# Kernel tuning notes

Measured on AMD Instinct MI355X. Metric: run time of the kernel, lower is better.

Reference implementation:

```python
import jax, jax.numpy as jnp
import numpy as np

N_CHARS = 256
EMB = 1024
HID = 2048
SEQ = 8192

def setup_inputs() -> dict:
    key = jax.random.key(0)
    ks = jax.random.split(key, 7)
    s = 0.02
    return {
        "input_seq": jax.random.randint(ks[0], (SEQ,), 0, N_CHARS),
        "emb": jax.random.normal(ks[1], (N_CHARS, EMB), jnp.float32) * s,
        "wax_w": jax.random.normal(ks[2], (HID, EMB), jnp.float32) * s,
        "wax_b": jnp.zeros((HID,), jnp.float32),
        "waa_w": jax.random.normal(ks[3], (HID, HID), jnp.float32) * s,
        "wya_w": jax.random.normal(ks[4], (N_CHARS, HID), jnp.float32) * s,
        "wya_b": jnp.zeros((N_CHARS,), jnp.float32),
    }

def reference(input_seq, emb, wax_w, wax_b, waa_w, wya_w, wya_b):
    # Embed whole sequence: [T, E]
    x_seq = emb[input_seq]
    # Precompute the input projection for all steps (parallel GEMM): [T, H]
    xa_seq = x_seq @ wax_w.T + wax_b

    def step(h, xa):
        h_new = jnp.tanh(xa + h @ waa_w.T)  # [H]
        o = h_new @ wya_w.T + wya_b          # [n_chars]
        return h_new, o

    h0 = jnp.zeros((HID,), x_seq.dtype)
    h_final, out = jax.lax.scan(step, h0, xa_seq)
    # out: [T, n_chars]; hidden returned as [1, H] to match torch module
    return out, h_final[None, :]
```

## Files before the change

### kernel.cpp

```cpp
#include <hip/hip_runtime.h>
#include <stdint.h>

#define SEQ 8192
#define EMB 1024
#define HID 2048
#define NCH 256

#define SCAN_B 128
#define SCAN_T 256
#define ROWS_PB (HID / SCAN_B)
#define SENT 0xFFFFFFFFu
#define NREP 4
#define NSLOT 8

typedef unsigned uint4v __attribute__((ext_vector_type(4)));

__global__ __launch_bounds__(256) void gemm_tn(const float* __restrict__ X,
                                               const float* __restrict__ W,
                                               const float* __restrict__ bias,
                                               float* __restrict__ C,
                                               int M, int N, int K)
{
    __shared__ float Xs[16][68];
    __shared__ float Ws[16][68];
    const int m0 = blockIdx.x * 64, n0 = blockIdx.y * 64;
    const int tid  = threadIdx.x;
    const int lrow = tid >> 2;
    const int kq   = (tid & 3) * 4;
    const int tx   = tid & 15, ty = tid >> 4;
    float acc[4][4] = {};
    const float* Xp = X + (size_t)(m0 + lrow) * K + kq;
    const float* Wp = W + (size_t)(n0 + lrow) * K + kq;

    for (int k0 = 0; k0 < K; k0 += 16) {
        float4 xv = *(const float4*)(Xp + k0);
        float4 wv = *(const float4*)(Wp + k0);
        __syncthreads();
        Xs[kq+0][lrow] = xv.x; Xs[kq+1][lrow] = xv.y;
        Xs[kq+2][lrow] = xv.z; Xs[kq+3][lrow] = xv.w;
        Ws[kq+0][lrow] = wv.x; Ws[kq+1][lrow] = wv.y;
        Ws[kq+2][lrow] = wv.z; Ws[kq+3][lrow] = wv.w;
        __syncthreads();
#pragma unroll
        for (int kk = 0; kk < 16; ++kk) {
            float4 av = *(const float4*)&Xs[kk][ty * 4];
            float4 bv = *(const float4*)&Ws[kk][tx * 4];
            float a[4] = {av.x, av.y, av.z, av.w};
            float b[4] = {bv.x, bv.y, bv.z, bv.w};
#pragma unroll
            for (int i = 0; i < 4; ++i)
#pragma unroll
                for (int j = 0; j < 4; ++j)
                    acc[i][j] += a[i] * b[j];
        }
    }
#pragma unroll
    for (int i = 0; i < 4; ++i) {
        const int m = m0 + ty * 4 + i;
#pragma unroll
        for (int j = 0; j < 4; ++j) {
            const int n = n0 + tx * 4 + j;
            C[(size_t)m * N + n] = acc[i][j] + bias[n];
        }
    }
}

__device__ __forceinline__ float fast_tanh(float x)
{
    float e = __builtin_amdgcn_exp2f(x * 2.885390081777927f);
    return 1.0f - 2.0f * __builtin_amdgcn_rcpf(e + 1.0f);
}

__global__ __launch_bounds__(SCAN_T, 1) void rnn_scan(
    const int*  __restrict__ seq,
    const float* __restrict__ waa,
    const float* __restrict__ P,
    float* __restrict__ H,
    unsigned* __restrict__ ring)
{
    const int b    = blockIdx.x;
    const int tid  = threadIdx.x;
    const int wv   = tid >> 6;
    const int lane = tid & 63;
    const int R0   = b * ROWS_PB + wv * 4;
    const int rep  = b & (NREP - 1);

    __shared__ float hbuf[2][HID];

    float w0[32], w1[32], w2[32], w3[32];
#pragma unroll
    for (int j = 0; j < 8; ++j) {
        const float* base = waa + 256 * j + 4 * lane;
        float4 a = *(const float4*)(base + (size_t)(R0 + 0) * HID);
        float4 c = *(const float4*)(base + (size_t)(R0 + 1) * HID);
        float4 d = *(const float4*)(base + (size_t)(R0 + 2) * HID);
        float4 e = *(const float4*)(base + (size_t)(R0 + 3) * HID);
        w0[4*j+0]=a.x; w0[4*j+1]=a.y; w0[4*j+2]=a.z; w0[4*j+3]=a.w;
        w1[4*j+0]=c.x; w1[4*j+1]=c.y; w1[4*j+2]=c.z; w1[4*j+3]=c.w;
        w2[4*j+0]=d.x; w2[4*j+1]=d.y; w2[4*j+2]=d.z; w2[4*j+3]=d.w;
        w3[4*j+0]=e.x; w3[4*j+1]=e.y; w3[4*j+2]=e.z; w3[4*j+3]=e.w;
    }
#pragma unroll
    for (int k = 0; k < 32; ++k) {
        asm volatile("" : "+v"(w0[k])); asm volatile("" : "+v"(w1[k]));
        asm volatile("" : "+v"(w2[k])); asm volatile("" : "+v"(w3[k]));
    }

    unsigned* myring = ring + (size_t)rep * NSLOT * HID;
    const uint4v SV = {SENT, SENT, SENT, SENT};
    uint4v v0 = SV, v1 = SV;

#pragma unroll 1
    for (int t = 0; t < SEQ; ++t) {
        const int ch = seq[t];
        float xav = 0.f;
        if (lane < 4) xav = P[(size_t)ch * HID + R0 + lane];

        asm volatile("s_waitcnt vmcnt(9)" : "+v"(v0), "+v"(v1) : : "memory");
        if (v0.x == SENT || v0.y == SENT || v0.z == SENT || v0.w == SENT ||
            v1.x == SENT || v1.y == SENT || v1.z == SENT || v1.w == SENT) {
            const unsigned* pp =
                myring + (size_t)(t & (NSLOT - 1)) * HID + tid * 8;
            do {
                asm volatile("s_waitcnt vmcnt(0)\n\t"
                             "global_load_dwordx4 %0, %2, off sc0 sc1\n\t"
                             "global_load_dwordx4 %1, %2, off offset:16 sc0 sc1\n\t"
                             "s_waitcnt vmcnt(0)"
                             : "+v"(v0), "+v"(v1) : "v"(pp) : "memory");
            } while (v0.x == SENT || v0.y == SENT || v0.z == SENT || v0.w == SENT ||
                     v1.x == SENT || v1.y == SENT || v1.z == SENT || v1.w == SENT);
        }
        *(uint4v*)&hbuf[t & 1][tid * 8]     = v0;
        *(uint4v*)&hbuf[t & 1][tid * 8 + 4] = v1;
        __syncthreads();

        float a0 = 0.f, a1 = 0.f, a2 = 0.f, a3 = 0.f;
        const float* hb = &hbuf[t & 1][4 * lane];
#pragma unroll
        for (int j = 0; j < 8; ++j) {
            float4 hv = *(const float4*)(hb + 256 * j);
            a0 += w0[4*j+0]*hv.x + w0[4*j+1]*hv.y + w0[4*j+2]*hv.z + w0[4*j+3]*hv.w;
            a1 += w1[4*j+0]*hv.x + w1[4*j+1]*hv.y + w1[4*j+2]*hv.z + w1[4*j+3]*hv.w;
            a2 += w2[4*j+0]*hv.x + w2[4*j+1]*hv.y + w2[4*j+2]*hv.z + w2[4*j+3]*hv.w;
            a3 += w3[4*j+0]*hv.x + w3[4*j+1]*hv.y + w3[4*j+2]*hv.z + w3[4*j+3]*hv.w;
        }
        a0 += __shfl_xor(a0, 1, 64);
        a1 += __shfl_xor(a1, 1, 64);
        a2 += __shfl_xor(a2, 1, 64);
        a3 += __shfl_xor(a3, 1, 64);
        float m01 = (lane & 1) ? a1 : a0;
        float m23 = (lane & 1) ? a3 : a2;
        m01 += __shfl_xor(m01, 2, 64);
        m23 += __shfl_xor(m23, 2, 64);
        float m = (lane & 2) ? m23 : m01;
        m += __shfl_xor(m, 4, 64);
        m += __shfl_xor(m, 8, 64);
        m += __shfl_xor(m, 16, 64);
        m += __shfl_xor(m, 32, 64);

        if (t + 1 < SEQ) {
            const unsigned* pn =
                myring + (size_t)((t + 1) & (NSLOT - 1)) * HID + tid * 8;
            v0 = SV; v1 = SV;
            asm volatile("global_load_dwordx4 %0, %2, off sc0 sc1\n\t"
                         "global_load_dwordx4 %1, %2, off offset:16 sc0 sc1"
                         : "+v"(v0), "+v"(v1) : "v"(pn) : "memory");
        }

        if (lane < 4) {
            float hn = fast_tanh(xav + m);
            const unsigned hu = __float_as_uint(hn);
            const int row = R0 + lane;
            const int s1 = (t + 1) & (NSLOT - 1);
            const int s5 = (t + 5) & (NSLOT - 1);
#pragma unroll
            for (int r = 0; r < NREP; ++r)
                __hip_atomic_store(ring + ((size_t)r * NSLOT + s1) * HID + row,
                                   hu, __ATOMIC_RELAXED,
                                   __HIP_MEMORY_SCOPE_AGENT);
#pragma unroll
            for (int r = 0; r < NREP; ++r)
                __hip_atomic_store(ring + ((size_t)r * NSLOT + s5) * HID + row,
                                   SENT, __ATOMIC_RELAXED,
                                   __HIP_MEMORY_SCOPE_AGENT);
            H[(size_t)(t + 1) * HID + row] = hn;
        }
    }
}

__global__ void copy_h(const float* __restrict__ src, float* __restrict__ dst)
{
    int i = blockIdx.x * blockDim.x + threadIdx.x;
    if (i < HID) dst[i] = src[i];
}

extern "C" void kernel_launch(void* const* d_in, const int* in_sizes, int n_in,
                              void* d_out, int out_size, void* d_ws, size_t ws_size,
                              hipStream_t stream)
{
    const int*   seq  = (const int*)  d_in[0];
    const float* emb  = (const float*)d_in[1];
    const float* wax  = (const float*)d_in[2];
    const float* waxb = (const float*)d_in[3];
    const float* waa  = (const float*)d_in[4];
    const float* wya  = (const float*)d_in[5];
    const float* wyab = (const float*)d_in[6];
    float* out = (float*)d_out;

    float*    H    = (float*)d_ws;
    float*    P    = (float*)((char*)d_ws + (size_t)(SEQ + 1) * HID * sizeof(float));
    unsigned* ring = (unsigned*)(P + (size_t)NCH * HID);

    (void)hipMemsetAsync(ring, 0xFF, (size_t)NREP * NSLOT * HID * sizeof(unsigned), stream);
    for (int r = 0; r < NREP; ++r)
        (void)hipMemsetAsync(ring + (size_t)r * NSLOT * HID, 0,
                             HID * sizeof(unsigned), stream);

    dim3 gA(NCH / 64, HID / 64);
    gemm_tn<<<gA, 256, 0, stream>>>(emb, wax, waxb, P, NCH, HID, EMB);

    rnn_scan<<<SCAN_B, SCAN_T, 0, stream>>>(seq, waa, P, H, ring);

    dim3 gC(SEQ / 64, NCH / 64);
    gemm_tn<<<gC, 256, 0, stream>>>(H + HID, wya, wyab, out, SEQ, NCH, HID);

    copy_h<<<(HID + 255) / 256, 256, 0, stream>>>(H + (size_t)SEQ * HID,
                                                  out + (size_t)SEQ * NCH);
}
```

Baseline: 18.86 ms.

## Use 64 blocks of 512 threads with per-wave LDS flags instead of barrier

Halves the number of scan blocks and doubles threads per block. Each thread now polls one 16-byte chunk of the ring. The block-wide __syncthreads is replaced by per-wave LDS readiness flags that consumers spin on chunk by chunk. The speculative prefetch of the next step's hidden state is removed. This aims to cut cross-block synchronization fan-in and barrier latency, but it gives up load overlap and adds LDS spin polling. It also relies on LDS ordering across waves without a formal fence.

Measured after the change: 15.62 ms. 1.21x faster.

```diff
diff --git a/kernel.cpp b/kernel.cpp
--- a/kernel.cpp
+++ b/kernel.cpp
@@ -6,8 +6,8 @@
 #define HID 2048
 #define NCH 256
 
-#define SCAN_B 128
-#define SCAN_T 256
+#define SCAN_B 64
+#define SCAN_T 512
 #define ROWS_PB (HID / SCAN_B)
 #define SENT 0xFFFFFFFFu
 #define NREP 4
@@ -71,7 +71,7 @@
     return 1.0f - 2.0f * __builtin_amdgcn_rcpf(e + 1.0f);
 }
 
-__global__ __launch_bounds__(SCAN_T, 1) void rnn_scan(
+__global__ __launch_bounds__(SCAN_T, 2) void rnn_scan(
     const int*  __restrict__ seq,
     const float* __restrict__ waa,
     const float* __restrict__ P,
@@ -86,6 +86,7 @@
     const int rep  = b & (NREP - 1);
 
     __shared__ float hbuf[2][HID];
+    __shared__ int   flg[2][8];
 
     float w0[32], w1[32], w2[32], w3[32];
 #pragma unroll
@@ -106,9 +107,10 @@
         asm volatile("" : "+v"(w2[k])); asm volatile("" : "+v"(w3[k]));
     }
 
+    if (tid < 16) ((int*)flg)[tid] = -1;
+    __syncthreads();
+
     unsigned* myring = ring + (size_t)rep * NSLOT * HID;
-    const uint4v SV = {SENT, SENT, SENT, SENT};
-    uint4v v0 = SV, v1 = SV;
 
 #pragma unroll 1
     for (int t = 0; t < SEQ; ++t) {
@@ -116,28 +118,24 @@
         float xav = 0.f;
         if (lane < 4) xav = P[(size_t)ch * HID + R0 + lane];
 
-        asm volatile("s_waitcnt vmcnt(9)" : "+v"(v0), "+v"(v1) : : "memory");
-        if (v0.x == SENT || v0.y == SENT || v0.z == SENT || v0.w == SENT ||
-            v1.x == SENT || v1.y == SENT || v1.z == SENT || v1.w == SENT) {
-            const unsigned* pp =
-                myring + (size_t)(t & (NSLOT - 1)) * HID + tid * 8;
-            do {
-                asm volatile("s_waitcnt vmcnt(0)\n\t"
-                             "global_load_dwordx4 %0, %2, off sc0 sc1\n\t"
-                             "global_load_dwordx4 %1, %2, off offset:16 sc0 sc1\n\t"
-                             "s_waitcnt vmcnt(0)"
-                             : "+v"(v0), "+v"(v1) : "v"(pp) : "memory");
-            } while (v0.x == SENT || v0.y == SENT || v0.z == SENT || v0.w == SENT ||
-                     v1.x == SENT || v1.y == SENT || v1.z == SENT || v1.w == SENT);
-        }
-        *(uint4v*)&hbuf[t & 1][tid * 8]     = v0;
-        *(uint4v*)&hbuf[t & 1][tid * 8 + 4] = v1;
-        __syncthreads();
+        uint4v v;
+        const unsigned* pp = myring + (size_t)(t & (NSLOT - 1)) * HID + tid * 4;
+        do {
+            asm volatile("global_load_dwordx4 %0, %1, off sc0 sc1\n\t"
+                         "s_waitcnt vmcnt(0)"
+                         : "=v"(v) : "v"(pp) : "memory");
+        } while (v.x == SENT || v.y == SENT || v.z == SENT || v.w == SENT);
+        *(uint4v*)&hbuf[t & 1][tid * 4] = v;
+
+        asm volatile("s_waitcnt lgkmcnt(0)" ::: "memory");
+        if (lane == 0) *(volatile int*)&flg[t & 1][wv] = t;
 
         float a0 = 0.f, a1 = 0.f, a2 = 0.f, a3 = 0.f;
         const float* hb = &hbuf[t & 1][4 * lane];
 #pragma unroll
         for (int j = 0; j < 8; ++j) {
+            while (*(volatile int*)&flg[t & 1][j] != t) { }
+            asm volatile("" ::: "memory");
             float4 hv = *(const float4*)(hb + 256 * j);
             a0 += w0[4*j+0]*hv.x + w0[4*j+1]*hv.y + w0[4*j+2]*hv.z + w0[4*j+3]*hv.w;
             a1 += w1[4*j+0]*hv.x + w1[4*j+1]*hv.y + w1[4*j+2]*hv.z + w1[4*j+3]*hv.w;
@@ -158,15 +156,6 @@
         m += __shfl_xor(m, 16, 64);
         m += __shfl_xor(m, 32, 64);
 
-        if (t + 1 < SEQ) {
-            const unsigned* pn =
-                myring + (size_t)((t + 1) & (NSLOT - 1)) * HID + tid * 8;
-            v0 = SV; v1 = SV;
-            asm volatile("global_load_dwordx4 %0, %2, off sc0 sc1\n\t"
-                         "global_load_dwordx4 %1, %2, off offset:16 sc0 sc1"
-                         : "+v"(v0), "+v"(v1) : "v"(pn) : "memory");
-        }
-
         if (lane < 4) {
             float hn = fast_tanh(xav + m);
             const unsigned hu = __float_as_uint(hn);
```
